# Kernel optimization log

Measured on AMD Instinct MI355X. Metric: run time of the kernel, lower is better.

Reference implementation:

```python
import jax, jax.numpy as jnp
import numpy as np
import math

B, S, E, H = 8, 1024, 512, 8
EPS = 1e-5

def _ln(x, g, b):
    mu = jnp.mean(x, axis=-1, keepdims=True)
    var = jnp.mean(jnp.square(x - mu), axis=-1, keepdims=True)
    return (x - mu) * jax.lax.rsqrt(var + EPS) * g + b

def setup_inputs() -> dict:
    key = jax.random.key(0)
    ks = iter(jax.random.split(key, 40))
    def w(shape, scale=0.02):
        return jax.random.normal(next(ks), shape, dtype=jnp.float32) * scale
    inp = {
        'x': jax.random.normal(next(ks), (B, S, E), dtype=jnp.float32),
        'cond': jax.random.normal(next(ks), (B, 1, E), dtype=jnp.float32),
        # AdaLN modulation linears (stored as (in,out))
        'g1w': w((E, E)), 'g1b': jnp.zeros((E,), jnp.float32),
        'be1w': w((E, E)), 'be1b': jnp.zeros((E,), jnp.float32),
        'a1w': w((E, E)), 'a1b': jnp.zeros((E,), jnp.float32),
        'g2w': w((E, E)), 'g2b': jnp.zeros((E,), jnp.float32),
        'be2w': w((E, E)), 'be2b': jnp.zeros((E,), jnp.float32),
        'a2w': w((E, E)), 'a2b': jnp.zeros((E,), jnp.float32),
        # LayerNorm affine
        'ln1g': jnp.ones((E,), jnp.float32), 'ln1b': jnp.zeros((E,), jnp.float32),
        'ln2g': jnp.ones((E,), jnp.float32), 'ln2b': jnp.zeros((E,), jnp.float32),
        # attention projections: each head has width E -> out dim H*E
        'wq': w((E, H * E)), 'bq': jnp.zeros((H * E,), jnp.float32),
        'wk': w((E, H * E)), 'bk': jnp.zeros((H * E,), jnp.float32),
        'wv': w((E, H * E)), 'bv': jnp.zeros((H * E,), jnp.float32),
        'lvw': w((H * E, E)), 'lvb': jnp.zeros((E,), jnp.float32),
        # FFN
        'f1w': w((E, 4 * E)), 'f1b': jnp.zeros((4 * E,), jnp.float32),
        'f2w': w((4 * E, E)), 'f2b': jnp.zeros((E,), jnp.float32),
    }
    return inp

def reference(x, cond, g1w, g1b, be1w, be1b, a1w, a1b, g2w, g2b, be2w, be2b, a2w, a2b,
              ln1g, ln1b, ln2g, ln2b, wq, bq, wk, bk, wv, bv, lvw, lvb, f1w, f1b, f2w, f2b):
    # AdaLN modulation signals, each (B,1,E)
    gamma1 = cond @ g1w + g1b
    beta1 = cond @ be1w + be1b
    alpha1 = cond @ a1w + a1b
    gamma2 = cond @ g2w + g2b
    beta2 = cond @ be2w + be2b
    alpha2 = cond @ a2w + a2b

    y = _ln(x, ln1g, ln1b) * (1.0 + gamma1) + beta1
    q = (y @ wq + bq).reshape(B, S, H, E).transpose(0, 2, 1, 3)  # (B,H,S,E)
    k = (y @ wk + bk).reshape(B, S, H, E).transpose(0, 2, 1, 3)
    v = (y @ wv + bv).reshape(B, S, H, E).transpose(0, 2, 1, 3)
    # NOTE: original scales by sqrt(q.size(2)) == sqrt(seq_len), not head_dim
    scale = 1.0 / math.sqrt(S)
    attn = jax.nn.softmax(jnp.einsum('bhse,bhte->bhst', q, k) * scale, axis=-1)
    o = jnp.einsum('bhst,bhte->bhse', attn, v)  # (B,H,S,E)
    o = o.transpose(0, 2, 1, 3).reshape(B, S, H * E)
    y = x + (o @ lvw + lvb) * alpha1

    z = _ln(y, ln2g, ln2b) * (1.0 + gamma2) + beta2
    z = (jax.nn.relu(z @ f1w + f1b) @ f2w + f2b) * alpha2
    return y + z
```

## Files before the change

kernel.cpp:

```cpp
#include <hip/hip_runtime.h>
#include <hip/hip_bf16.h>

typedef __bf16 bf16_t;
typedef bf16_t bf16x8 __attribute__((ext_vector_type(8)));
typedef bf16_t bf16x4 __attribute__((ext_vector_type(4)));
typedef float f32x4 __attribute__((ext_vector_type(4)));

typedef const __attribute__((address_space(1))) void GV;
typedef __attribute__((address_space(3))) void LV;

__device__ __forceinline__ void gload_lds16(const bf16_t* gsrc, bf16_t* ldst) {
    __builtin_amdgcn_global_load_lds((GV*)gsrc, (LV*)ldst, 16, 0, 0);
}

__global__ __launch_bounds__(256) void wtrans_kernel(const float* __restrict__ in,
                                                     bf16_t* __restrict__ out, int K, int N)
{
    __shared__ float tile[32][33];
    const int n0 = blockIdx.x * 32, k0 = blockIdx.y * 32;
    const int tx = threadIdx.x & 31, ty = threadIdx.x >> 5;
#pragma unroll
    for (int i = 0; i < 32; i += 8)
        tile[ty + i][tx] = in[(long long)(k0 + ty + i) * N + n0 + tx];
    __syncthreads();
#pragma unroll
    for (int i = 0; i < 32; i += 8)
        out[(long long)(n0 + ty + i) * K + k0 + tx] = (bf16_t)tile[tx][ty + i];
}

__global__ __launch_bounds__(256) void modsig_kernel(
    const float* __restrict__ cond,
    const float* __restrict__ w0, const float* __restrict__ w1, const float* __restrict__ w2,
    const float* __restrict__ w3, const float* __restrict__ w4, const float* __restrict__ w5,
    const float* __restrict__ c0, const float* __restrict__ c1, const float* __restrict__ c2,
    const float* __restrict__ c3, const float* __restrict__ c4, const float* __restrict__ c5,
    float* __restrict__ out)
{
    __shared__ float cs[512];
    const int sig = blockIdx.x >> 3, b = blockIdx.x & 7;
    const float* w; const float* bi;
    switch (sig) {
        case 0: w = w0; bi = c0; break;
        case 1: w = w1; bi = c1; break;
        case 2: w = w2; bi = c2; break;
        case 3: w = w3; bi = c3; break;
        case 4: w = w4; bi = c4; break;
        default: w = w5; bi = c5; break;
    }
    for (int i = threadIdx.x; i < 512; i += 256) cs[i] = cond[b * 512 + i];
    __syncthreads();
    for (int n = threadIdx.x; n < 512; n += 256) {
        float s = bi[n];
        for (int i = 0; i < 512; ++i) s = fmaf(cs[i], w[(long long)i * 512 + n], s);
        out[(long long)(sig * 8 + b) * 512 + n] = s;
    }
}

__global__ __launch_bounds__(128) void ln_mod_kernel(
    const float* __restrict__ x, const float* __restrict__ g, const float* __restrict__ be,
    const float* __restrict__ gamma, const float* __restrict__ beta, bf16_t* __restrict__ out)
{
    const int row = blockIdx.x;
    const int b = row >> 10;
    const int t = threadIdx.x;
    const float4 v = reinterpret_cast<const float4*>(x + (long long)row * 512)[t];
    float s = v.x + v.y + v.z + v.w;
    float ss = v.x * v.x + v.y * v.y + v.z * v.z + v.w * v.w;
    for (int o = 32; o; o >>= 1) { s += __shfl_xor(s, o); ss += __shfl_xor(ss, o); }
    __shared__ float red[4];
    if ((t & 63) == 0) { red[t >> 6] = s; red[2 + (t >> 6)] = ss; }
    __syncthreads();
    s = red[0] + red[1]; ss = red[2] + red[3];
    const float mu = s * (1.f / 512.f);
    const float rstd = rsqrtf(ss * (1.f / 512.f) - mu * mu + 1e-5f);
    const float4 gv = reinterpret_cast<const float4*>(g)[t];
    const float4 bv = reinterpret_cast<const float4*>(be)[t];
    const float4 ga = reinterpret_cast<const float4*>(gamma + b * 512)[t];
    const float4 bb = reinterpret_cast<const float4*>(beta + b * 512)[t];
    bf16x4 ov;
    ov[0] = (bf16_t)(((v.x - mu) * rstd * gv.x + bv.x) * (1.f + ga.x) + bb.x);
    ov[1] = (bf16_t)(((v.y - mu) * rstd * gv.y + bv.y) * (1.f + ga.y) + bb.y);
    ov[2] = (bf16_t)(((v.z - mu) * rstd * gv.z + bv.z) * (1.f + ga.z) + bb.z);
    ov[3] = (bf16_t)(((v.w - mu) * rstd * gv.w + bv.w) * (1.f + ga.w) + bb.w);
    reinterpret_cast<bf16x4*>(out + (long long)row * 512)[t] = ov;
}

template <int EPI>
__global__ __launch_bounds__(256) void gemm128_kernel(
    const bf16_t* __restrict__ A, const bf16_t* __restrict__ B,
    const float* __restrict__ bias, void* Cout,
    int M, int N, int K, int lda, int ldb, int ldc)
{
    const int nbx = gridDim.x;
    const int lin = blockIdx.y * nbx + blockIdx.x;
    const int cpx = (nbx * gridDim.y) >> 3;
    const int swz = (lin & 7) * cpx + (lin >> 3);
    const int m0 = (swz / nbx) * 128, n0 = (swz % nbx) * 128;
    const int tid = threadIdx.x, lane = tid & 63, wid = tid >> 6;
    const int wr = wid >> 1, wc = wid & 1;

    __shared__ bf16_t As[8192];
    __shared__ bf16_t Bs[8192];

    f32x4 acc[4][4];
#pragma unroll
    for (int m = 0; m < 4; ++m)
#pragma unroll
        for (int n = 0; n < 4; ++n) acc[m][n] = (f32x4){0.f, 0.f, 0.f, 0.f};

    const int r8 = lane >> 3;
    const int lc = (lane & 7) ^ r8;
    long long aOff[4], bOff[4];
#pragma unroll
    for (int i = 0; i < 4; ++i) {
        const int row = i * 32 + wid * 8 + r8;
        aOff[i] = (long long)(m0 + row) * lda + lc * 8;
        bOff[i] = (long long)(n0 + row) * ldb + lc * 8;
    }

    const int frow = lane & 15, lg = lane >> 4;
    const int p0 = lg ^ (frow & 7);

    for (int kt = 0; kt < K; kt += 64) {
#pragma unroll
        for (int i = 0; i < 4; ++i) gload_lds16(A + aOff[i] + kt, As + i * 2048 + wid * 512);
#pragma unroll
        for (int i = 0; i < 4; ++i) gload_lds16(B + bOff[i] + kt, Bs + i * 2048 + wid * 512);
        __syncthreads();
        __builtin_amdgcn_s_setprio(1);
#pragma unroll
        for (int kk = 0; kk < 2; ++kk) {
            const int pc = p0 ^ (kk << 2);
            bf16x8 af[4], bfv[4];
#pragma unroll
            for (int m = 0; m < 4; ++m)
                af[m] = *reinterpret_cast<const bf16x8*>(As + (wr * 64 + m * 16 + frow) * 64 + pc * 8);
#pragma unroll
            for (int n = 0; n < 4; ++n)
                bfv[n] = *reinterpret_cast<const bf16x8*>(Bs + (wc * 64 + n * 16 + frow) * 64 + pc * 8);
#pragma unroll
            for (int m = 0; m < 4; ++m)
#pragma unroll
                for (int n = 0; n < 4; ++n)
                    acc[m][n] = __builtin_amdgcn_mfma_f32_16x16x32_bf16(af[m], bfv[n], acc[m][n], 0, 0, 0);
        }
        __builtin_amdgcn_s_setprio(0);
        __syncthreads();
    }

#pragma unroll
    for (int m = 0; m < 4; ++m) {
        const int gm = m0 + wr * 64 + m * 16 + ((lane >> 4) << 2);
#pragma unroll
        for (int n = 0; n < 4; ++n) {
            const int gn = n0 + wc * 64 + n * 16 + (lane & 15);
            const float bb = bias ? bias[gn] : 0.f;
#pragma unroll
            for (int j = 0; j < 4; ++j) {
                const float v = acc[m][n][j] + bb;
                const int gmj = gm + j;
                if (EPI == 0) {
                    ((bf16_t*)Cout)[(long long)gmj * ldc + gn] = (bf16_t)v;
                } else {
                    ((bf16_t*)Cout)[(long long)gmj * ldc + gn] = (bf16_t)fmaxf(v, 0.f);
                }
            }
        }
    }
}

__global__ __launch_bounds__(256) void gemmqkv_kernel(
    const bf16_t* __restrict__ A, const bf16_t* __restrict__ B,
    const float* __restrict__ bq, const float* __restrict__ bk, const float* __restrict__ bv,
    bf16_t* __restrict__ qkv, bf16_t* __restrict__ vtb)
{
    const int lin = blockIdx.y * 96 + blockIdx.x;
    const int swz = (lin & 7) * 768 + (lin >> 3);
    const int m0 = (swz / 96) * 128, n0 = (swz % 96) * 128;
    const int sec = n0 >> 12;
    const float* bias = (sec == 0) ? bq : ((sec == 1) ? bk : bv);
    const int tid = threadIdx.x, lane = tid & 63, wid = tid >> 6;
    const int wr = wid >> 1, wc = wid & 1;

    __shared__ bf16_t As[8192];
    __shared__ bf16_t Bs[8192];

    f32x4 acc[4][4];
#pragma unroll
    for (int m = 0; m < 4; ++m)
#pragma unroll
        for (int n = 0; n < 4; ++n) acc[m][n] = (f32x4){0.f, 0.f, 0.f, 0.f};

    const int r8 = lane >> 3;
    const int lc = (lane & 7) ^ r8;
    long long aOff[4], bOff[4];
#pragma unroll
    for (int i = 0; i < 4; ++i) {
        const int row = i * 32 + wid * 8 + r8;
        aOff[i] = (long long)(m0 + row) * 512 + lc * 8;
        bOff[i] = (long long)(n0 + row) * 512 + lc * 8;
    }

    const int frow = lane & 15, lg = lane >> 4;
    const int p0 = lg ^ (frow & 7);

    for (int kt = 0; kt < 512; kt += 64) {
#pragma unroll
        for (int i = 0; i < 4; ++i) gload_lds16(A + aOff[i] + kt, As + i * 2048 + wid * 512);
#pragma unroll
        for (int i = 0; i < 4; ++i) gload_lds16(B + bOff[i] + kt, Bs + i * 2048 + wid * 512);
        __syncthreads();
        __builtin_amdgcn_s_setprio(1);
#pragma unroll
        for (int kk = 0; kk < 2; ++kk) {
            const int pc = p0 ^ (kk << 2);
            bf16x8 af[4], bfv[4];
#pragma unroll
            for (int m = 0; m < 4; ++m)
                af[m] = *reinterpret_cast<const bf16x8*>(As + (wr * 64 + m * 16 + frow) * 64 + pc * 8);
#pragma unroll
            for (int n = 0; n < 4; ++n)
                bfv[n] = *reinterpret_cast<const bf16x8*>(Bs + (wc * 64 + n * 16 + frow) * 64 + pc * 8);
#pragma unroll
            for (int m = 0; m < 4; ++m)
#pragma unroll
                for (int n = 0; n < 4; ++n)
                    acc[m][n] = __builtin_amdgcn_mfma_f32_16x16x32_bf16(af[m], bfv[n], acc[m][n], 0, 0, 0);
        }
        __builtin_amdgcn_s_setprio(0);
        __syncthreads();
    }

#pragma unroll
    for (int m = 0; m < 4; ++m) {
        const int gm = m0 + wr * 64 + m * 16 + ((lane >> 4) << 2);
#pragma unroll
        for (int n = 0; n < 4; ++n) {
            const int gn = n0 + wc * 64 + n * 16 + (lane & 15);
            const int gnl = gn & 4095;
            const float bb = bias[gnl];
#pragma unroll
            for (int j = 0; j < 4; ++j) {
                const float v = acc[m][n][j] + bb;
                const int gmj = gm + j;
                if (sec < 2) {
                    qkv[(long long)sec * 33554432 + (long long)gmj * 4096 + gnl] = (bf16_t)v;
                } else {
                    const long long ci =
                        (long long)(((gmj >> 10) * 8 + (gnl >> 9)) * 512 + (gnl & 511)) * 1024 + (gmj & 1023);
                    vtb[ci] = (bf16_t)v;
                }
            }
        }
    }
}

__global__ __launch_bounds__(256) void gemm64_kernel(
    const bf16_t* __restrict__ A, const bf16_t* __restrict__ B,
    const float* __restrict__ bias, float* __restrict__ Cout,
    const float* __restrict__ resid, const float* __restrict__ alpha,
    int M, int N, int K, int lda, int ldb)
{
    const int nbx = gridDim.x;
    const int lin = blockIdx.y * nbx + blockIdx.x;
    const int cpx = (nbx * gridDim.y) >> 3;
    const int swz = (lin & 7) * cpx + (lin >> 3);
    const int m0 = (swz / nbx) * 64, n0 = (swz % nbx) * 128;
    const int tid = threadIdx.x, lane = tid & 63, wid = tid >> 6;
    const int wr = wid >> 1, wc = wid & 1;

    __shared__ bf16_t As[4096];
    __shared__ bf16_t Bs[8192];

    f32x4 acc[2][4];
#pragma unroll
    for (int m = 0; m < 2; ++m)
#pragma unroll
        for (int n = 0; n < 4; ++n) acc[m][n] = (f32x4){0.f, 0.f, 0.f, 0.f};

    const int r8 = lane >> 3;
    const int lc = (lane & 7) ^ r8;
    long long aOff[2], bOff[4];
#pragma unroll
    for (int i = 0; i < 2; ++i)
        aOff[i] = (long long)(m0 + i * 32 + wid * 8 + r8) * lda + lc * 8;
#pragma unroll
    for (int i = 0; i < 4; ++i)
        bOff[i] = (long long)(n0 + i * 32 + wid * 8 + r8) * ldb + lc * 8;

    const int frow = lane & 15, lg = lane >> 4;
    const int p0 = lg ^ (frow & 7);

    for (int kt = 0; kt < K; kt += 64) {
#pragma unroll
        for (int i = 0; i < 2; ++i) gload_lds16(A + aOff[i] + kt, As + i * 2048 + wid * 512);
#pragma unroll
        for (int i = 0; i < 4; ++i) gload_lds16(B + bOff[i] + kt, Bs + i * 2048 + wid * 512);
        __syncthreads();
        __builtin_amdgcn_s_setprio(1);
#pragma unroll
        for (int kk = 0; kk < 2; ++kk) {
            const int pc = p0 ^ (kk << 2);
            bf16x8 af[2], bfv[4];
#pragma unroll
            for (int m = 0; m < 2; ++m)
                af[m] = *reinterpret_cast<const bf16x8*>(As + (wr * 32 + m * 16 + frow) * 64 + pc * 8);
#pragma unroll
            for (int n = 0; n < 4; ++n)
                bfv[n] = *reinterpret_cast<const bf16x8*>(Bs + (wc * 64 + n * 16 + frow) * 64 + pc * 8);
#pragma unroll
            for (int m = 0; m < 2; ++m)
#pragma unroll
                for (int n = 0; n < 4; ++n)
                    acc[m][n] = __builtin_amdgcn_mfma_f32_16x16x32_bf16(af[m], bfv[n], acc[m][n], 0, 0, 0);
        }
        __builtin_amdgcn_s_setprio(0);
        __syncthreads();
    }

#pragma unroll
    for (int m = 0; m < 2; ++m) {
        const int gm = m0 + wr * 32 + m * 16 + ((lane >> 4) << 2);
#pragma unroll
        for (int n = 0; n < 4; ++n) {
            const int gn = n0 + wc * 64 + n * 16 + (lane & 15);
            const float bb = bias[gn];
#pragma unroll
            for (int j = 0; j < 4; ++j) {
                const int gmj = gm + j;
                const long long ci = (long long)gmj * 512 + gn;
                Cout[ci] = resid[ci] + (acc[m][n][j] + bb) * alpha[(gmj >> 10) * 512 + gn];
            }
        }
    }
}

#define FA_LDS 68608
#define SCL 0.04508422132207354f
__global__ __launch_bounds__(256, 2) void flash_kernel(
    bf16_t* __restrict__ qb, const bf16_t* __restrict__ kb, const bf16_t* __restrict__ vtb)
{
    extern __shared__ char smem[];
    bf16_t* Ks = (bf16_t*)smem;
    bf16_t* Vs = (bf16_t*)(smem + 32768);
    char* PB = smem + 65536;
    float* pmaxB = (float*)(smem + 67584);
    float* psumB = (float*)(smem + 68096);

    const int bid = blockIdx.x;
    const int xcd = bid & 7, idx = bid >> 3;
    const int qt = idx & 31, bhl = idx >> 5;
    const int bh = xcd * 8 + bhl;
    const int b = bh >> 3, h = bh & 7;
    const int q0 = qt * 32;
    const int tid = threadIdx.x, lane = tid & 63, wid = tid >> 6;
    const int laneq = lane & 15, lx = lane & 7, lg = lane >> 4;
    const int wk = wid >> 1, wq = wid & 1;
    const int we = wid;

#pragma unroll
    for (int r = 0; r < 8; ++r) {
        const int row = r * 4 + wid;
        gload_lds16(kb + ((long long)(b * 1024 + row) * 8 + h) * 512 + ((lane ^ (row & 7)) << 3),
                    Ks + row * 512);
    }
    const int qi = wq * 16 + laneq;
    bf16x8 qfrag[16];
    {
        const bf16_t* qrow = qb + ((long long)(b * 1024 + q0 + qi) * 8 + h) * 512 + lg * 8;
#pragma unroll
        for (int ks = 0; ks < 16; ++ks) qfrag[ks] = *reinterpret_cast<const bf16x8*>(qrow + ks * 32);
    }
    f32x4 accA[8], accB[8];
#pragma unroll
    for (int e = 0; e < 8; ++e) { accA[e] = (f32x4){0.f,0.f,0.f,0.f}; accB[e] = (f32x4){0.f,0.f,0.f,0.f}; }
    float mS = 0.f, mPA = 0.f, mPB = 0.f, lA = 0.f, lB = 0.f;
    const int rA = wk * 16 + laneq;
    const int qA = laneq, qB = laneq + 16;
    __syncthreads();

    for (int t = 0; t < 32; ++t) {
#pragma unroll
        for (int r = 0; r < 8; ++r) {
            const int e0 = (r * 4 + wid) * 16;
            const int e = e0 + (lane >> 2);
            gload_lds16(vtb + ((long long)bh * 512 + e) * 1024 + t * 32 + (((lane & 3) ^ (e & 3)) << 3),
                        Vs + e0 * 32);
        }
        f32x4 s0 = (f32x4){0.f, 0.f, 0.f, 0.f};
        const char* KsB = (const char*)Ks;
        __builtin_amdgcn_s_setprio(1);
#pragma unroll
        for (int ks = 0; ks < 16; ++ks) {
            const int co = (((ks * 4 + lg) ^ lx) << 4);
            bf16x8 a0 = *(const bf16x8*)(KsB + rA * 1024 + co);
            s0 = __builtin_amdgcn_mfma_f32_16x16x32_bf16(a0, qfrag[ks], s0, 0, 0, 0);
        }
        __builtin_amdgcn_s_setprio(0);
        float f[4], pe[4];
#pragma unroll
        for (int j = 0; j < 4; ++j) f[j] = s0[j] * SCL;
        float mloc = fmaxf(fmaxf(f[0], f[1]), fmaxf(f[2], f[3]));
        mloc = fmaxf(mloc, __shfl_xor(mloc, 16));
        mloc = fmaxf(mloc, __shfl_xor(mloc, 32));
        float sl = 0.f;
#pragma unroll
        for (int j = 0; j < 4; ++j) { pe[j] = exp2f(f[j] - mS); sl += pe[j]; }
        sl += __shfl_xor(sl, 16);
        sl += __shfl_xor(sl, 32);
        if (lane < 16) {
            pmaxB[(t & 1) * 64 + wk * 32 + wq * 16 + lane] = mloc;
            psumB[(t & 1) * 64 + wk * 32 + wq * 16 + lane] = sl;
        }
        {
            bf16x4 p;
#pragma unroll
            for (int j = 0; j < 4; ++j) p[j] = (bf16_t)pe[j];
            const int g = wk * 4 + lg;
            *(bf16x4*)(PB + qi * 64 + (((g >> 1) ^ (qi & 3)) << 4) + ((g & 1) << 3)) = p;
        }
        __syncthreads();

        if (t < 31) {
#pragma unroll
            for (int r = 0; r < 8; ++r) {
                const int row = r * 4 + wid;
                gload_lds16(kb + ((long long)(b * 1024 + t * 32 + 32 + row) * 8 + h) * 512
                                + ((lane ^ (row & 7)) << 3),
                            Ks + row * 512);
            }
        }
        const char* VB = (const char*)Vs;
        bf16x8 pA = *(const bf16x8*)(PB + qA * 64 + ((lg ^ (qA & 3)) << 4));
        bf16x8 pBv = *(const bf16x8*)(PB + qB * 64 + ((lg ^ (qB & 3)) << 4));
        __builtin_amdgcn_s_setprio(1);
#pragma unroll
        for (int ef = 0; ef < 8; ++ef) {
            const int re = we * 128 + ef * 16 + laneq;
            bf16x8 av = *(const bf16x8*)(VB + re * 64 + ((lg ^ (re & 3)) << 4));
            accA[ef] = __builtin_amdgcn_mfma_f32_16x16x32_bf16(av, pA, accA[ef], 0, 0, 0);
            accB[ef] = __builtin_amdgcn_mfma_f32_16x16x32_bf16(av, pBv, accB[ef], 0, 0, 0);
        }
        __builtin_amdgcn_s_setprio(0);
        {
            const float* pmax_t = pmaxB + (t & 1) * 64;
            const float* psum_t = psumB + (t & 1) * 64;
            mS = fmaxf(mS, fmaxf(pmax_t[qi], pmax_t[32 + qi]));
            lA += psum_t[qA] + psum_t[32 + qA];
            lB += psum_t[qB] + psum_t[32 + qB];
            const float mnA = fmaxf(mPA, fmaxf(pmax_t[qA], pmax_t[32 + qA]));
            const float mnB = fmaxf(mPB, fmaxf(pmax_t[qB], pmax_t[32 + qB]));
            if (__ballot((mnA > mPA) || (mnB > mPB))) {
                const float rsA = exp2f(mPA - mnA), rsB = exp2f(mPB - mnB);
                lA *= rsA; lB *= rsB;
#pragma unroll
                for (int e = 0; e < 8; ++e) {
#pragma unroll
                    for (int j = 0; j < 4; ++j) { accA[e][j] *= rsA; accB[e][j] *= rsB; }
                }
            }
            mPA = mnA; mPB = mnB;
        }
        __syncthreads();
    }

    const float iA = 1.f / lA, iB = 1.f / lB;
#pragma unroll
    for (int ef = 0; ef < 8; ++ef) {
        const int e0 = we * 128 + ef * 16 + lg * 4;
        bf16x4 oA, oB;
#pragma unroll
        for (int j = 0; j < 4; ++j) { oA[j] = (bf16_t)(accA[ef][j] * iA); oB[j] = (bf16_t)(accB[ef][j] * iB); }
        *(bf16x4*)(qb + ((long long)(b * 1024 + q0 + qA) * 8 + h) * 512 + e0) = oA;
        *(bf16x4*)(qb + ((long long)(b * 1024 + q0 + qB) * 8 + h) * 512 + e0) = oB;
    }
}

extern "C" void kernel_launch(void* const* d_in, const int* in_sizes, int n_in,
                              void* d_out, int out_size, void* d_ws, size_t ws_size,
                              hipStream_t stream)
{
    const float* x    = (const float*)d_in[0];
    const float* cond = (const float*)d_in[1];
    const float* g1w  = (const float*)d_in[2];  const float* g1b  = (const float*)d_in[3];
    const float* be1w = (const float*)d_in[4];  const float* be1b = (const float*)d_in[5];
    const float* a1w  = (const float*)d_in[6];  const float* a1b  = (const float*)d_in[7];
    const float* g2w  = (const float*)d_in[8];  const float* g2b  = (const float*)d_in[9];
    const float* be2w = (const float*)d_in[10]; const float* be2b = (const float*)d_in[11];
    const float* a2w  = (const float*)d_in[12]; const float* a2b  = (const float*)d_in[13];
    const float* ln1g = (const float*)d_in[14]; const float* ln1b = (const float*)d_in[15];
    const float* ln2g = (const float*)d_in[16]; const float* ln2b = (const float*)d_in[17];
    const float* wq   = (const float*)d_in[18]; const float* bq   = (const float*)d_in[19];
    const float* wk   = (const float*)d_in[20]; const float* bk   = (const float*)d_in[21];
    const float* wv   = (const float*)d_in[22]; const float* bv   = (const float*)d_in[23];
    const float* lvw  = (const float*)d_in[24]; const float* lvb  = (const float*)d_in[25];
    const float* f1w  = (const float*)d_in[26]; const float* f1b  = (const float*)d_in[27];
    const float* f2w  = (const float*)d_in[28]; const float* f2b  = (const float*)d_in[29];
    (void)in_sizes; (void)n_in; (void)out_size; (void)ws_size;

    char* w8 = (char*)d_ws;
    float*  mod  = (float*)(w8);
    bf16_t* wqT  = (bf16_t*)(w8 + 98304);
    bf16_t* lvwT = (bf16_t*)(w8 + 98304 + 3 * 4194304);
    bf16_t* f1wT = (bf16_t*)(w8 + 98304 + 4 * 4194304);
    bf16_t* f2wT = (bf16_t*)(w8 + 98304 + 4 * 4194304 + 2097152);
    bf16_t* ybf  = (bf16_t*)(w8 + 98304 + 4 * 4194304 + 2 * 2097152);
    bf16_t* qb   = (bf16_t*)(w8 + 98304 + 4 * 4194304 + 2 * 2097152 + 8388608);
    bf16_t* kb   = qb + 33554432;
    bf16_t* vtb  = kb + 33554432;

    (void)hipFuncSetAttribute((const void*)flash_kernel,
                              hipFuncAttributeMaxDynamicSharedMemorySize, FA_LDS);

    const dim3 blk(256);
    wtrans_kernel<<<dim3(128, 16), blk, 0, stream>>>(wq, wqT, 512, 4096);
    wtrans_kernel<<<dim3(128, 16), blk, 0, stream>>>(wk, wqT + 2097152, 512, 4096);
    wtrans_kernel<<<dim3(128, 16), blk, 0, stream>>>(wv, wqT + 2 * 2097152, 512, 4096);
    wtrans_kernel<<<dim3(16, 128), blk, 0, stream>>>(lvw, lvwT, 4096, 512);
    wtrans_kernel<<<dim3(64, 16), blk, 0, stream>>>(f1w, f1wT, 512, 2048);
    wtrans_kernel<<<dim3(16, 64), blk, 0, stream>>>(f2w, f2wT, 2048, 512);
    modsig_kernel<<<48, blk, 0, stream>>>(cond, g1w, be1w, a1w, g2w, be2w, a2w,
                                          g1b, be1b, a1b, g2b, be2b, a2b, mod);
    ln_mod_kernel<<<8192, 128, 0, stream>>>(x, ln1g, ln1b, mod, mod + 4096, ybf);
    gemmqkv_kernel<<<dim3(96, 64), blk, 0, stream>>>(ybf, wqT, bq, bk, bv, qb, vtb);
    flash_kernel<<<2048, 256, FA_LDS, stream>>>(qb, kb, vtb);
    gemm64_kernel<<<dim3(4, 128), blk, 0, stream>>>(qb, lvwT, lvb, (float*)d_out, x, mod + 8192,
        8192, 512, 4096, 4096, 4096);
    ln_mod_kernel<<<8192, 128, 0, stream>>>((const float*)d_out, ln2g, ln2b,
                                            mod + 12288, mod + 16384, ybf);
    gemm128_kernel<1><<<dim3(16, 64), blk, 0, stream>>>(ybf, f1wT, f1b, qb,
        8192, 2048, 512, 512, 512, 2048);
    gemm64_kernel<<<dim3(4, 128), blk, 0, stream>>>(qb, f2wT, f2b, (float*)d_out,
        (const float*)d_out, mod + 20480,
        8192, 512, 2048, 2048, 2048);
}
```

Baseline: 675.8 us.

## Double-buffer GEMM LDS tiles, merge weight transposes, unroll modsig accumulation

Converts the three GEMM kernels (gemm128, gemmqkv, gemm64) to double-buffered LDS. The next K-tile is prefetched with global_load_lds while the current one feeds the MFMAs, and one of the two barriers per iteration is dropped. The six weight-transpose launches are merged into a single kernel that dispatches on block index, removing launch overhead. The modsig dot product is split across four independent accumulators to break the serial FMA chain. Doubling the LDS footprint may lower occupancy, and the fp32 summation order in modsig changes slightly.

```diff
diff --git a/kernel.cpp b/kernel.cpp
--- a/kernel.cpp
+++ b/kernel.cpp
@@ -13,11 +13,29 @@
     __builtin_amdgcn_global_load_lds((GV*)gsrc, (LV*)ldst, 16, 0, 0);
 }
 
-__global__ __launch_bounds__(256) void wtrans_kernel(const float* __restrict__ in,
-                                                     bf16_t* __restrict__ out, int K, int N)
+__global__ __launch_bounds__(256) void wtrans_all_kernel(
+    const float* __restrict__ wq, const float* __restrict__ wk, const float* __restrict__ wv,
+    const float* __restrict__ lvw, const float* __restrict__ f1w, const float* __restrict__ f2w,
+    bf16_t* __restrict__ wqT, bf16_t* __restrict__ lvwT,
+    bf16_t* __restrict__ f1wT, bf16_t* __restrict__ f2wT)
 {
     __shared__ float tile[32][33];
-    const int n0 = blockIdx.x * 32, k0 = blockIdx.y * 32;
+    const int bid = blockIdx.x;
+    const float* in; bf16_t* out; int K, N, nx, local;
+    if (bid < 6144) {
+        const int sec = bid >> 11;
+        local = bid & 2047;
+        in = (sec == 0) ? wq : ((sec == 1) ? wk : wv);
+        out = wqT + (long long)sec * 2097152;
+        K = 512; N = 4096; nx = 128;
+    } else if (bid < 8192) {
+        local = bid - 6144; in = lvw; out = lvwT; K = 4096; N = 512; nx = 16;
+    } else if (bid < 9216) {
+        local = bid - 8192; in = f1w; out = f1wT; K = 512; N = 2048; nx = 64;
+    } else {
+        local = bid - 9216; in = f2w; out = f2wT; K = 2048; N = 512; nx = 16;
+    }
+    const int n0 = (local % nx) * 32, k0 = (local / nx) * 32;
     const int tx = threadIdx.x & 31, ty = threadIdx.x >> 5;
 #pragma unroll
     for (int i = 0; i < 32; i += 8)
@@ -50,9 +68,14 @@
     for (int i = threadIdx.x; i < 512; i += 256) cs[i] = cond[b * 512 + i];
     __syncthreads();
     for (int n = threadIdx.x; n < 512; n += 256) {
-        float s = bi[n];
-        for (int i = 0; i < 512; ++i) s = fmaf(cs[i], w[(long long)i * 512 + n], s);
-        out[(long long)(sig * 8 + b) * 512 + n] = s;
+        float s0 = 0.f, s1 = 0.f, s2 = 0.f, s3 = 0.f;
+        for (int i = 0; i < 512; i += 4) {
+            s0 = fmaf(cs[i], w[(long long)i * 512 + n], s0);
+            s1 = fmaf(cs[i + 1], w[(long long)(i + 1) * 512 + n], s1);
+            s2 = fmaf(cs[i + 2], w[(long long)(i + 2) * 512 + n], s2);
+            s3 = fmaf(cs[i + 3], w[(long long)(i + 3) * 512 + n], s3);
+        }
+        out[(long long)(sig * 8 + b) * 512 + n] = bi[n] + (s0 + s1) + (s2 + s3);
     }
 }
 
@@ -99,8 +122,8 @@
     const int tid = threadIdx.x, lane = tid & 63, wid = tid >> 6;
     const int wr = wid >> 1, wc = wid & 1;
 
-    __shared__ bf16_t As[8192];
-    __shared__ bf16_t Bs[8192];
+    __shared__ bf16_t As[16384];
+    __shared__ bf16_t Bs[16384];
 
     f32x4 acc[4][4];
 #pragma unroll
@@ -121,12 +144,23 @@
     const int frow = lane & 15, lg = lane >> 4;
     const int p0 = lg ^ (frow & 7);
 
+#pragma unroll
+    for (int i = 0; i < 4; ++i) gload_lds16(A + aOff[i], As + i * 2048 + wid * 512);
+#pragma unroll
+    for (int i = 0; i < 4; ++i) gload_lds16(B + bOff[i], Bs + i * 2048 + wid * 512);
+
     for (int kt = 0; kt < K; kt += 64) {
-#pragma unroll
-        for (int i = 0; i < 4; ++i) gload_lds16(A + aOff[i] + kt, As + i * 2048 + wid * 512);
-#pragma unroll
-        for (int i = 0; i < 4; ++i) gload_lds16(B + bOff[i] + kt, Bs + i * 2048 + wid * 512);
+        const int cur = (kt >> 6) & 1;
         __syncthreads();
+        if (kt + 64 < K) {
+            const int nxt = (cur ^ 1) * 8192;
+#pragma unroll
+            for (int i = 0; i < 4; ++i) gload_lds16(A + aOff[i] + kt + 64, As + nxt + i * 2048 + wid * 512);
+#pragma unroll
+            for (int i = 0; i < 4; ++i) gload_lds16(B + bOff[i] + kt + 64, Bs + nxt + i * 2048 + wid * 512);
+        }
+        const bf16_t* Ab = As + cur * 8192;
+        const bf16_t* Bb = Bs + cur * 8192;
         __builtin_amdgcn_s_setprio(1);
 #pragma unroll
         for (int kk = 0; kk < 2; ++kk) {
@@ -134,10 +168,10 @@
             bf16x8 af[4], bfv[4];
 #pragma unroll
             for (int m = 0; m < 4; ++m)
-                af[m] = *reinterpret_cast<const bf16x8*>(As + (wr * 64 + m * 16 + frow) * 64 + pc * 8);
+                af[m] = *reinterpret_cast<const bf16x8*>(Ab + (wr * 64 + m * 16 + frow) * 64 + pc * 8);
 #pragma unroll
             for (int n = 0; n < 4; ++n)
-                bfv[n] = *reinterpret_cast<const bf16x8*>(Bs + (wc * 64 + n * 16 + frow) * 64 + pc * 8);
+                bfv[n] = *reinterpret_cast<const bf16x8*>(Bb + (wc * 64 + n * 16 + frow) * 64 + pc * 8);
 #pragma unroll
             for (int m = 0; m < 4; ++m)
 #pragma unroll
@@ -145,7 +179,6 @@
                     acc[m][n] = __builtin_amdgcn_mfma_f32_16x16x32_bf16(af[m], bfv[n], acc[m][n], 0, 0, 0);
         }
         __builtin_amdgcn_s_setprio(0);
-        __syncthreads();
     }
 
 #pragma unroll
@@ -182,8 +215,8 @@
     const int tid = threadIdx.x, lane = tid & 63, wid = tid >> 6;
     const int wr = wid >> 1, wc = wid & 1;
 
-    __shared__ bf16_t As[8192];
-    __shared__ bf16_t Bs[8192];
+    __shared__ bf16_t As[16384];
+    __shared__ bf16_t Bs[16384];
 
     f32x4 acc[4][4];
 #pragma unroll
@@ -204,12 +237,23 @@
     const int frow = lane & 15, lg = lane >> 4;
     const int p0 = lg ^ (frow & 7);
 
+#pragma unroll
+    for (int i = 0; i < 4; ++i) gload_lds16(A + aOff[i], As + i * 2048 + wid * 512);
+#pragma unroll
+    for (int i = 0; i < 4; ++i) gload_lds16(B + bOff[i], Bs + i * 2048 + wid * 512);
+
     for (int kt = 0; kt < 512; kt += 64) {
-#pragma unroll
-        for (int i = 0; i < 4; ++i) gload_lds16(A + aOff[i] + kt, As + i * 2048 + wid * 512);
-#pragma unroll
-        for (int i = 0; i < 4; ++i) gload_lds16(B + bOff[i] + kt, Bs + i * 2048 + wid * 512);
+        const int cur = (kt >> 6) & 1;
         __syncthreads();
+        if (kt + 64 < 512) {
+            const int nxt = (cur ^ 1) * 8192;
+#pragma unroll
+            for (int i = 0; i < 4; ++i) gload_lds16(A + aOff[i] + kt + 64, As + nxt + i * 2048 + wid * 512);
+#pragma unroll
+            for (int i = 0; i < 4; ++i) gload_lds16(B + bOff[i] + kt + 64, Bs + nxt + i * 2048 + wid * 512);
+        }
+        const bf16_t* Ab = As + cur * 8192;
+        const bf16_t* Bb = Bs + cur * 8192;
         __builtin_amdgcn_s_setprio(1);
 #pragma unroll
         for (int kk = 0; kk < 2; ++kk) {
@@ -217,10 +261,10 @@
             bf16x8 af[4], bfv[4];
 #pragma unroll
             for (int m = 0; m < 4; ++m)
-                af[m] = *reinterpret_cast<const bf16x8*>(As + (wr * 64 + m * 16 + frow) * 64 + pc * 8);
+                af[m] = *reinterpret_cast<const bf16x8*>(Ab + (wr * 64 + m * 16 + frow) * 64 + pc * 8);
 #pragma unroll
             for (int n = 0; n < 4; ++n)
-                bfv[n] = *reinterpret_cast<const bf16x8*>(Bs + (wc * 64 + n * 16 + frow) * 64 + pc * 8);
+                bfv[n] = *reinterpret_cast<const bf16x8*>(Bb + (wc * 64 + n * 16 + frow) * 64 + pc * 8);
 #pragma unroll
             for (int m = 0; m < 4; ++m)
 #pragma unroll
@@ -228,7 +272,6 @@
                     acc[m][n] = __builtin_amdgcn_mfma_f32_16x16x32_bf16(af[m], bfv[n], acc[m][n], 0, 0, 0);
         }
         __builtin_amdgcn_s_setprio(0);
-        __syncthreads();
     }
 
 #pragma unroll
@@ -269,8 +312,8 @@
     const int tid = threadIdx.x, lane = tid & 63, wid = tid >> 6;
     const int wr = wid >> 1, wc = wid & 1;
 
-    __shared__ bf16_t As[4096];
-    __shared__ bf16_t Bs[8192];
+    __shared__ bf16_t As[8192];
+    __shared__ bf16_t Bs[16384];
 
     f32x4 acc[2][4];
 #pragma unroll
@@ -291,12 +334,24 @@
     const int frow = lane & 15, lg = lane >> 4;
     const int p0 = lg ^ (frow & 7);
 
+#pragma unroll
+    for (int i = 0; i < 2; ++i) gload_lds16(A + aOff[i], As + i * 2048 + wid * 512);
+#pragma unroll
+    for (int i = 0; i < 4; ++i) gload_lds16(B + bOff[i], Bs + i * 2048 + wid * 512);
+
     for (int kt = 0; kt < K; kt += 64) {
-#pragma unroll
-        for (int i = 0; i < 2; ++i) gload_lds16(A + aOff[i] + kt, As + i * 2048 + wid * 512);
-#pragma unroll
-        for (int i = 0; i < 4; ++i) gload_lds16(B + bOff[i] + kt, Bs + i * 2048 + wid * 512);
+        const int cur = (kt >> 6) & 1;
         __syncthreads();
+        if (kt + 64 < K) {
+#pragma unroll
+            for (int i = 0; i < 2; ++i)
+                gload_lds16(A + aOff[i] + kt + 64, As + (cur ^ 1) * 4096 + i * 2048 + wid * 512);
+#pragma unroll
+            for (int i = 0; i < 4; ++i)
+                gload_lds16(B + bOff[i] + kt + 64, Bs + (cur ^ 1) * 8192 + i * 2048 + wid * 512);
+        }
+        const bf16_t* Ab = As + cur * 4096;
+        const bf16_t* Bb = Bs + cur * 8192;
         __builtin_amdgcn_s_setprio(1);
 #pragma unroll
         for (int kk = 0; kk < 2; ++kk) {
@@ -304,10 +359,10 @@
             bf16x8 af[2], bfv[4];
 #pragma unroll
             for (int m = 0; m < 2; ++m)
-                af[m] = *reinterpret_cast<const bf16x8*>(As + (wr * 32 + m * 16 + frow) * 64 + pc * 8);
+                af[m] = *reinterpret_cast<const bf16x8*>(Ab + (wr * 32 + m * 16 + frow) * 64 + pc * 8);
 #pragma unroll
             for (int n = 0; n < 4; ++n)
-                bfv[n] = *reinterpret_cast<const bf16x8*>(Bs + (wc * 64 + n * 16 + frow) * 64 + pc * 8);
+                bfv[n] = *reinterpret_cast<const bf16x8*>(Bb + (wc * 64 + n * 16 + frow) * 64 + pc * 8);
 #pragma unroll
             for (int m = 0; m < 2; ++m)
 #pragma unroll
@@ -315,7 +370,6 @@
                     acc[m][n] = __builtin_amdgcn_mfma_f32_16x16x32_bf16(af[m], bfv[n], acc[m][n], 0, 0, 0);
         }
         __builtin_amdgcn_s_setprio(0);
-        __syncthreads();
     }
 
 #pragma unroll
@@ -513,12 +567,8 @@
                               hipFuncAttributeMaxDynamicSharedMemorySize, FA_LDS);
 
     const dim3 blk(256);
-    wtrans_kernel<<<dim3(128, 16), blk, 0, stream>>>(wq, wqT, 512, 4096);
-    wtrans_kernel<<<dim3(128, 16), blk, 0, stream>>>(wk, wqT + 2097152, 512, 4096);
-    wtrans_kernel<<<dim3(128, 16), blk, 0, stream>>>(wv, wqT + 2 * 2097152, 512, 4096);
-    wtrans_kernel<<<dim3(16, 128), blk, 0, stream>>>(lvw, lvwT, 4096, 512);
-    wtrans_kernel<<<dim3(64, 16), blk, 0, stream>>>(f1w, f1wT, 512, 2048);
-    wtrans_kernel<<<dim3(16, 64), blk, 0, stream>>>(f2w, f2wT, 2048, 512);
+    wtrans_all_kernel<<<10240, blk, 0, stream>>>(wq, wk, wv, lvw, f1w, f2w,
+                                                 wqT, lvwT, f1wT, f2wT);
     modsig_kernel<<<48, blk, 0, stream>>>(cond, g1w, be1w, a1w, g2w, be2w, a2w,
                                           g1b, be1b, a1b, g2b, be2b, a2b, mod);
     ln_mod_kernel<<<8192, 128, 0, stream>>>(x, ln1g, ln1b, mod, mod + 4096, ybf);
```

New measurement: 678.9 us. Within noise of the previous version (+0.5%).
